# Kernel optimization log

Measured on AMD Instinct MI355X. Metric: run time of the kernel, lower is better.

## Reference

```python
import jax, jax.numpy as jnp
import numpy as np

B, TQ, TK, D = 16, 1024, 4096, 512


def setup_inputs() -> dict:
    key = jax.random.key(0)
    k1, k2, k3 = jax.random.split(key, 3)
    decoder_output = jax.random.normal(k1, (B, TQ, D), dtype=jnp.float32)
    encoder_output = jax.random.normal(k2, (B, TK, D), dtype=jnp.float32)
    # Keras Dense(lstm_size): kernel [D, D] (glorot-ish scale), bias [D] (zeros init)
    W_a = jax.random.normal(k3, (D, D), dtype=jnp.float32) * (1.0 / np.sqrt(D))
    b_a = jnp.zeros((D,), dtype=jnp.float32)
    return {"decoder_output": decoder_output, "encoder_output": encoder_output,
            "W_a": W_a, "b_a": b_a}


def reference(decoder_output, encoder_output, W_a, b_a):
    # Luong 'general' attention:
    # proj = Dense(encoder_output)            [B, Tk, D]
    proj = jnp.einsum('bkd,de->bke', encoder_output, W_a) + b_a
    # score = dec @ proj^T                    [B, Tq, Tk]
    score = jnp.einsum('bqd,bkd->bqk', decoder_output, proj)
    # softmax over encoder time axis (tf axis=2 == last axis here)
    alignment_vector = jax.nn.softmax(score, axis=-1)
    # context = align @ encoder_output        [B, Tq, D]
    context_vector = jnp.einsum('bqk,bkd->bqd', alignment_vector, encoder_output)
    return (context_vector, alignment_vector)
```

## Files before the change

kernel.cpp:

```cpp
#include <hip/hip_runtime.h>
#include <hip/hip_bf16.h>

#define B_  16
#define TQ_ 1024
#define TK_ 4096
#define D_  512

typedef unsigned short u16;
typedef __attribute__((ext_vector_type(8))) short short8;
typedef __attribute__((ext_vector_type(8))) _Float16 f16x8;
typedef __attribute__((ext_vector_type(4))) float f32x4;

__device__ __forceinline__ u16 bf16_rne(float x) {
  unsigned u = __float_as_uint(x);
  u += 0x7FFFu + ((u >> 16) & 1u);
  return (u16)(u >> 16);
}
__device__ __forceinline__ float bf16_as_f32(u16 h) {
  return __uint_as_float(((unsigned)h) << 16);
}
__device__ __forceinline__ void split_bf16(float x, u16& h, u16& l) {
  u16 hh = bf16_rne(x);
  h = hh;
  l = bf16_rne(x - bf16_as_f32(hh));
}

__device__ __forceinline__ void glld16(const void* g, void* lds) {
  __builtin_amdgcn_global_load_lds(
      (const __attribute__((address_space(1))) unsigned int*)g,
      (__attribute__((address_space(3))) unsigned int*)lds, 16, 0, 0);
}

__device__ __forceinline__ int seg_src(int l) {
  return (l & 3) ^ ((l >> 2) & 3) ^ ((l >> 4) & 3);
}

__global__ __launch_bounds__(256) void transpose_conv_kernel(
    const float* __restrict__ E, _Float16* __restrict__ ET,
    _Float16* __restrict__ EF)
{
  __shared__ float tile[64][65];
  const int b  = blockIdx.z;
  const int k0 = blockIdx.x * 64;
  const int d0 = blockIdx.y * 64;
  const float* Eb = E + (long long)b * TK_ * D_;
  _Float16* ETb = ET + (long long)b * D_ * TK_;

  const int t  = threadIdx.x;
  const int r  = t >> 2;
  const int c4 = (t & 3) * 16;

  __align__(16) _Float16 g[16];
  #pragma unroll
  for (int i = 0; i < 16; i += 4) {
    float4 v = *(const float4*)&Eb[(long long)(k0 + r) * D_ + d0 + c4 + i];
    tile[r][c4 + i + 0] = v.x;
    tile[r][c4 + i + 1] = v.y;
    tile[r][c4 + i + 2] = v.z;
    tile[r][c4 + i + 3] = v.w;
    g[i + 0] = (_Float16)v.x;
    g[i + 1] = (_Float16)v.y;
    g[i + 2] = (_Float16)v.z;
    g[i + 3] = (_Float16)v.w;
  }
  if (EF) {
    _Float16* EFb = EF + (long long)b * TK_ * D_;
    uint4* dstF = (uint4*)&EFb[(long long)(k0 + r) * D_ + d0 + c4];
    dstF[0] = ((const uint4*)g)[0];
    dstF[1] = ((const uint4*)g)[1];
  }
  __syncthreads();

  __align__(16) _Float16 h[16];
  #pragma unroll
  for (int i = 0; i < 16; ++i) h[i] = (_Float16)tile[c4 + i][r];
  uint4* dst = (uint4*)&ETb[(long long)(d0 + r) * TK_ + k0 + c4];
  dst[0] = ((const uint4*)h)[0];
  dst[1] = ((const uint4*)h)[1];
}

#define DBM 128
#define DBN 128
#define DBK 32
#define DPAD 40

__global__ __launch_bounds__(256) void gemm_dec2_kernel(
    const float* __restrict__ A, const float* __restrict__ Bm,
    _Float16* __restrict__ Ch, _Float16* __restrict__ Cl)
{
  __shared__ u16 Ah[DBM * DPAD];
  __shared__ u16 Al[DBM * DPAD];
  __shared__ u16 Bh[DBN * DPAD];
  __shared__ u16 Bl[DBN * DPAD];

  const float* Ab = A  + (long long)(blockIdx.y * DBM) * D_;
  const float* Bb = Bm + (long long)(blockIdx.x * DBN) * D_;

  const int t    = threadIdx.x;
  const int r    = t >> 1;
  const int hf   = t & 1;
  const int lane = t & 63;
  const int wave = t >> 6;
  const int wr   = (wave >> 1) * 64;
  const int wc   = (wave & 1) * 64;
  const int ln   = lane & 15;
  const int qd   = lane >> 4;

  f32x4 acc[4][4];
  #pragma unroll
  for (int i = 0; i < 4; ++i)
    #pragma unroll
    for (int j = 0; j < 4; ++j) { f32x4 z = {0.f,0.f,0.f,0.f}; acc[i][j] = z; }

  const float* srcA = Ab + (long long)r * D_ + hf * 16;
  const float* srcB = Bb + (long long)r * D_ + hf * 16;
  u16* dAh = &Ah[r * DPAD + hf * 16];
  u16* dAl = &Al[r * DPAD + hf * 16];
  u16* dBh = &Bh[r * DPAD + hf * 16];
  u16* dBl = &Bl[r * DPAD + hf * 16];

  for (int k0 = 0; k0 < D_; k0 += DBK) {
    {
      __align__(16) u16 h[16], l[16];
      #pragma unroll
      for (int i = 0; i < 16; i += 4) {
        float4 v = *(const float4*)(srcA + k0 + i);
        split_bf16(v.x, h[i+0], l[i+0]);
        split_bf16(v.y, h[i+1], l[i+1]);
        split_bf16(v.z, h[i+2], l[i+2]);
        split_bf16(v.w, h[i+3], l[i+3]);
      }
      ((uint4*)dAh)[0] = ((const uint4*)h)[0];
      ((uint4*)dAh)[1] = ((const uint4*)h)[1];
      ((uint4*)dAl)[0] = ((const uint4*)l)[0];
      ((uint4*)dAl)[1] = ((const uint4*)l)[1];
      #pragma unroll
      for (int i = 0; i < 16; i += 4) {
        float4 v = *(const float4*)(srcB + k0 + i);
        split_bf16(v.x, h[i+0], l[i+0]);
        split_bf16(v.y, h[i+1], l[i+1]);
        split_bf16(v.z, h[i+2], l[i+2]);
        split_bf16(v.w, h[i+3], l[i+3]);
      }
      ((uint4*)dBh)[0] = ((const uint4*)h)[0];
      ((uint4*)dBh)[1] = ((const uint4*)h)[1];
      ((uint4*)dBl)[0] = ((const uint4*)l)[0];
      ((uint4*)dBl)[1] = ((const uint4*)l)[1];
    }
    __syncthreads();

    short8 fah[4], fal[4], fbh[4], fbl[4];
    #pragma unroll
    for (int i = 0; i < 4; ++i) {
      int ra = (wr + i * 16 + ln) * DPAD + qd * 8;
      int rb = (wc + i * 16 + ln) * DPAD + qd * 8;
      fah[i] = *(const short8*)&Ah[ra];
      fal[i] = *(const short8*)&Al[ra];
      fbh[i] = *(const short8*)&Bh[rb];
      fbl[i] = *(const short8*)&Bl[rb];
    }
    #pragma unroll
    for (int i = 0; i < 4; ++i)
      #pragma unroll
      for (int j = 0; j < 4; ++j) {
        acc[i][j] = __builtin_amdgcn_mfma_f32_16x16x32_bf16(fah[i], fbh[j], acc[i][j], 0, 0, 0);
        acc[i][j] = __builtin_amdgcn_mfma_f32_16x16x32_bf16(fah[i], fbl[j], acc[i][j], 0, 0, 0);
        acc[i][j] = __builtin_amdgcn_mfma_f32_16x16x32_bf16(fal[i], fbh[j], acc[i][j], 0, 0, 0);
      }
    __syncthreads();
  }

  const int m0 = blockIdx.y * DBM;
  const int n0 = blockIdx.x * DBN;
  #pragma unroll
  for (int i = 0; i < 4; ++i)
    #pragma unroll
    for (int j = 0; j < 4; ++j)
      #pragma unroll
      for (int rg = 0; rg < 4; ++rg) {
        int row = m0 + wr + i * 16 + qd * 4 + rg;
        int col = n0 + wc + j * 16 + ln;
        float x = acc[i][j][rg];
        _Float16 h = (_Float16)x;
        _Float16 l = (_Float16)(x - (float)h);
        long long idx = (long long)row * D_ + col;
        Ch[idx] = h;
        Cl[idx] = l;
      }
}

#define SBM 128
#define SBN 128
#define SBK 32

template<bool F16B>
__global__ __launch_bounds__(256) void gemm_score_kernel(
    const _Float16* __restrict__ A_h, const _Float16* __restrict__ A_l,
    const float* __restrict__ Bf, const _Float16* __restrict__ B16,
    float* __restrict__ C)
{
  __shared__ _Float16 sAh[SBM * SBK];
  __shared__ _Float16 sAl[SBM * SBK];
  __shared__ _Float16 sB [SBN * SBK];

  const int bz = blockIdx.z;
  const int m0 = blockIdx.y * SBM;
  const int n0 = blockIdx.x * SBN;
  const _Float16* Ahb = A_h + (long long)bz * TQ_ * D_ + (long long)m0 * D_;
  const _Float16* Alb = A_l + (long long)bz * TQ_ * D_ + (long long)m0 * D_;

  const int t    = threadIdx.x;
  const int lane = t & 63;
  const int wave = t >> 6;
  const int wr   = (wave >> 1) * 64;
  const int wc   = (wave & 1) * 64;
  const int ln   = lane & 15;
  const int qd   = lane >> 4;
  const int sw   = qd ^ (ln & 3) ^ (ln >> 2);

  f32x4 acc[4][4];
  #pragma unroll
  for (int i = 0; i < 4; ++i)
    #pragma unroll
    for (int j = 0; j < 4; ++j) { f32x4 z = {0.f,0.f,0.f,0.f}; acc[i][j] = z; }

  const int c0   = wave * 2;
  const int arow = c0 * 16 + (lane >> 2);
  const int ab   = seg_src(lane) * 16;
  const char* gAh = (const char*)Ahb + (long long)arow * D_ * 2 + ab;
  const char* gAl = (const char*)Alb + (long long)arow * D_ * 2 + ab;
  const long long rstep = (long long)16 * D_ * 2;
  char* lAh = (char*)sAh + c0 * 1024 + lane * 16;
  char* lAl = (char*)sAl + c0 * 1024 + lane * 16;
  char* lB  = (char*)sB  + c0 * 1024 + lane * 16;

  const char* gB16 = nullptr;
  if constexpr (F16B) {
    const _Float16* Bb16 = B16 + (long long)bz * TK_ * D_ + (long long)n0 * D_;
    gB16 = (const char*)Bb16 + (long long)arow * D_ * 2 + ab;
  }

  const float* Bb = Bf + (long long)bz * TK_ * D_ + (long long)n0 * D_;
  const int brow = t >> 1;
  const int bhf  = t & 1;
  const float* srcB = Bb + (long long)brow * D_ + bhf * 16;
  const int bh2 = (brow & 3) ^ ((brow >> 2) & 3);
  _Float16* dB0 = &sB[brow * SBK + ((2 * bhf    ) ^ bh2) * 8];
  _Float16* dB1 = &sB[brow * SBK + ((2 * bhf + 1) ^ bh2) * 8];

  for (int k0 = 0; k0 < D_; k0 += SBK) {
    glld16(gAh + (long long)k0 * 2, lAh);
    glld16(gAh + (long long)k0 * 2 + rstep, lAh + 1024);
    glld16(gAl + (long long)k0 * 2, lAl);
    glld16(gAl + (long long)k0 * 2 + rstep, lAl + 1024);
    if constexpr (F16B) {
      glld16(gB16 + (long long)k0 * 2, lB);
      glld16(gB16 + (long long)k0 * 2 + rstep, lB + 1024);
    } else {
      __align__(16) _Float16 hb[16];
      #pragma unroll
      for (int i = 0; i < 16; i += 4) {
        float4 v = *(const float4*)(srcB + k0 + i);
        hb[i+0] = (_Float16)v.x;
        hb[i+1] = (_Float16)v.y;
        hb[i+2] = (_Float16)v.z;
        hb[i+3] = (_Float16)v.w;
      }
      *(uint4*)dB0 = ((const uint4*)hb)[0];
      *(uint4*)dB1 = ((const uint4*)hb)[1];
    }
    __syncthreads();

    f16x8 fah[4], fal[4], fb[4];
    #pragma unroll
    for (int i = 0; i < 4; ++i) {
      int ra = (wr + i * 16 + ln) * SBK + sw * 8;
      int rb = (wc + i * 16 + ln) * SBK + sw * 8;
      fah[i] = *(const f16x8*)&sAh[ra];
      fal[i] = *(const f16x8*)&sAl[ra];
      fb[i]  = *(const f16x8*)&sB[rb];
    }
    #pragma unroll
    for (int i = 0; i < 4; ++i)
      #pragma unroll
      for (int j = 0; j < 4; ++j) {
        acc[i][j] = __builtin_amdgcn_mfma_f32_16x16x32_f16(fah[i], fb[j], acc[i][j], 0, 0, 0);
        acc[i][j] = __builtin_amdgcn_mfma_f32_16x16x32_f16(fal[i], fb[j], acc[i][j], 0, 0, 0);
      }
    __syncthreads();
  }

  float* Cb = C + (long long)bz * TQ_ * TK_;
  #pragma unroll
  for (int i = 0; i < 4; ++i)
    #pragma unroll
    for (int j = 0; j < 4; ++j)
      #pragma unroll
      for (int rg = 0; rg < 4; ++rg) {
        int row = m0 + wr + i * 16 + qd * 4 + rg;
        int col = n0 + wc + j * 16 + ln;
        Cb[(long long)row * TK_ + col] = acc[i][j][rg];
      }
}

template<bool WP16>
__global__ __launch_bounds__(256) void softmax_kernel(
    float* __restrict__ P, _Float16* __restrict__ P16)
{
  __shared__ float red[8];
  float* p = P + (long long)blockIdx.x * TK_;
  const int t    = threadIdx.x;
  const int lane = t & 63;
  const int wave = t >> 6;

  float4 v[4];
  float mx = -3.0e38f;
  #pragma unroll
  for (int i = 0; i < 4; ++i) {
    v[i] = *(const float4*)&p[i * 1024 + t * 4];
    mx = fmaxf(mx, fmaxf(fmaxf(v[i].x, v[i].y), fmaxf(v[i].z, v[i].w)));
  }
  #pragma unroll
  for (int o = 32; o > 0; o >>= 1) mx = fmaxf(mx, __shfl_xor(mx, o, 64));
  if (lane == 0) red[wave] = mx;
  __syncthreads();
  mx = fmaxf(fmaxf(red[0], red[1]), fmaxf(red[2], red[3]));

  float s = 0.f;
  #pragma unroll
  for (int i = 0; i < 4; ++i) {
    v[i].x = __expf(v[i].x - mx);
    v[i].y = __expf(v[i].y - mx);
    v[i].z = __expf(v[i].z - mx);
    v[i].w = __expf(v[i].w - mx);
    s += (v[i].x + v[i].y) + (v[i].z + v[i].w);
  }
  #pragma unroll
  for (int o = 32; o > 0; o >>= 1) s += __shfl_xor(s, o, 64);
  if (lane == 0) red[4 + wave] = s;
  __syncthreads();
  s = (red[4] + red[5]) + (red[6] + red[7]);
  const float inv = 1.0f / s;

  _Float16* p16 = WP16 ? (P16 + (long long)blockIdx.x * TK_) : nullptr;
  #pragma unroll
  for (int i = 0; i < 4; ++i) {
    v[i].x *= inv; v[i].y *= inv; v[i].z *= inv; v[i].w *= inv;
    *(float4*)&p[i * 1024 + t * 4] = v[i];
    if constexpr (WP16) {
      union { _Float16 h[4]; uint2 u; } pk;
      pk.h[0] = (_Float16)v[i].x;
      pk.h[1] = (_Float16)v[i].y;
      pk.h[2] = (_Float16)v[i].z;
      pk.h[3] = (_Float16)v[i].w;
      *(uint2*)&p16[i * 1024 + t * 4] = pk.u;
    }
  }
}

#define CBM 64
#define CBN 256
#define CBK 32

template<bool F16A>
__global__ __launch_bounds__(512) void gemm_ctx_kernel(
    const float* __restrict__ P, const _Float16* __restrict__ P16,
    const _Float16* __restrict__ ET, float* __restrict__ C)
{
  __shared__ _Float16 sA[CBM * CBK];
  __shared__ _Float16 sB[CBN * CBK];

  const int bz = blockIdx.z;
  const int m0 = blockIdx.y * CBM;
  const int n0 = blockIdx.x * CBN;
  const float*    Pb = P  + (long long)bz * TQ_ * TK_ + (long long)m0 * TK_;
  const _Float16* Eb = ET + (long long)bz * D_ * TK_  + (long long)n0 * TK_;

  const int t    = threadIdx.x;
  const int lane = t & 63;
  const int wave = t >> 6;
  const int wr   = (wave >> 2) * 32;
  const int wc   = (wave & 3) * 64;
  const int ln   = lane & 15;
  const int qd   = lane >> 4;
  const int sw   = qd ^ (ln & 3) ^ (ln >> 2);

  f32x4 acc[2][4];
  #pragma unroll
  for (int i = 0; i < 2; ++i)
    #pragma unroll
    for (int j = 0; j < 4; ++j) { f32x4 z = {0.f,0.f,0.f,0.f}; acc[i][j] = z; }

  const int c0   = wave * 2;
  const int brow = c0 * 16 + (lane >> 2);
  const int bb   = seg_src(lane) * 16;
  const char* gB = (const char*)Eb + (long long)brow * TK_ * 2 + bb;
  const long long rstep = (long long)16 * TK_ * 2;
  char* lB = (char*)sB + c0 * 1024 + lane * 16;

  const char* gA16 = nullptr;
  char* lA16 = nullptr;
  if constexpr (F16A) {
    const _Float16* Pb16 = P16 + (long long)bz * TQ_ * TK_ + (long long)m0 * TK_;
    const int acrow = wave * 16 + (lane >> 2);
    gA16 = (const char*)Pb16 + (long long)acrow * TK_ * 2 + bb;
    lA16 = (char*)sA + wave * 1024 + lane * 16;
  }
  const int arow = t >> 3;
  const int aseg = t & 7;
  const float* gA = Pb + (long long)arow * TK_ + aseg * 4;
  const int ah2 = (arow & 3) ^ ((arow >> 2) & 3);
  _Float16* lA = &sA[arow * CBK + (((aseg >> 1) ^ ah2) * 8) + (aseg & 1) * 4];

  for (int k0 = 0; k0 < TK_; k0 += CBK) {
    glld16(gB + (long long)k0 * 2, lB);
    glld16(gB + (long long)k0 * 2 + rstep, lB + 1024);
    if constexpr (F16A) {
      if (wave < 4) glld16(gA16 + (long long)k0 * 2, lA16);
    } else {
      float4 v = *(const float4*)(gA + k0);
      union { _Float16 h[4]; uint2 u; } pk;
      pk.h[0] = (_Float16)v.x;
      pk.h[1] = (_Float16)v.y;
      pk.h[2] = (_Float16)v.z;
      pk.h[3] = (_Float16)v.w;
      *(uint2*)lA = pk.u;
    }
    __syncthreads();

    f16x8 fa[2], fb[4];
    #pragma unroll
    for (int i = 0; i < 2; ++i)
      fa[i] = *(const f16x8*)&sA[(wr + i * 16 + ln) * CBK + sw * 8];
    #pragma unroll
    for (int j = 0; j < 4; ++j)
      fb[j] = *(const f16x8*)&sB[(wc + j * 16 + ln) * CBK + sw * 8];
    #pragma unroll
    for (int i = 0; i < 2; ++i)
      #pragma unroll
      for (int j = 0; j < 4; ++j)
        acc[i][j] = __builtin_amdgcn_mfma_f32_16x16x32_f16(fa[i], fb[j], acc[i][j], 0, 0, 0);
    __syncthreads();
  }

  float* Cb = C + (long long)bz * TQ_ * D_;
  #pragma unroll
  for (int i = 0; i < 2; ++i)
    #pragma unroll
    for (int j = 0; j < 4; ++j)
      #pragma unroll
      for (int rg = 0; rg < 4; ++rg) {
        int row = m0 + wr + i * 16 + qd * 4 + rg;
        int col = n0 + wc + j * 16 + ln;
        Cb[(long long)row * D_ + col] = acc[i][j][rg];
      }
}

extern "C" void kernel_launch(void* const* d_in, const int* in_sizes, int n_in,
                              void* d_out, int out_size, void* d_ws, size_t ws_size,
                              hipStream_t stream) {
  (void)in_sizes; (void)n_in; (void)out_size;
  const float* dec = (const float*)d_in[0];
  const float* enc = (const float*)d_in[1];
  const float* Wa  = (const float*)d_in[2];

  float* ctx   = (float*)d_out;
  float* align = ctx + (long long)B_ * TQ_ * D_;

  char* ws = (char*)d_ws;
  const size_t SZ_ENCT = (size_t)B_ * D_ * TK_ * 2;
  const size_t SZ_DEC2 = (size_t)B_ * TQ_ * D_ * 2;
  const size_t SZ_ENCF = (size_t)B_ * TK_ * D_ * 2;
  const size_t SZ_P16  = (size_t)B_ * TQ_ * TK_ * 2;

  _Float16* encT  = (_Float16*)(ws);
  _Float16* dec2h = (_Float16*)(ws + SZ_ENCT);
  _Float16* dec2l = (_Float16*)(ws + SZ_ENCT + SZ_DEC2);
  _Float16* encF  = (_Float16*)(ws + SZ_ENCT + 2 * SZ_DEC2);
  _Float16* p16   = (_Float16*)(ws + SZ_ENCT);

  const bool mid  = ws_size >= SZ_ENCT + 2 * SZ_DEC2 + SZ_ENCF;
  const bool full = ws_size >= SZ_ENCT + SZ_P16;

  transpose_conv_kernel<<<dim3(TK_ / 64, D_ / 64, B_), 256, 0, stream>>>(
      enc, encT, mid ? encF : nullptr);

  gemm_dec2_kernel<<<dim3(D_ / DBN, (B_ * TQ_) / DBM, 1), 256, 0, stream>>>(
      dec, Wa, dec2h, dec2l);

  if (mid)
    gemm_score_kernel<true><<<dim3(TK_ / SBN, TQ_ / SBM, B_), 256, 0, stream>>>(
        dec2h, dec2l, enc, encF, align);
  else
    gemm_score_kernel<false><<<dim3(TK_ / SBN, TQ_ / SBM, B_), 256, 0, stream>>>(
        dec2h, dec2l, enc, nullptr, align);

  if (full)
    softmax_kernel<true><<<B_ * TQ_, 256, 0, stream>>>(align, p16);
  else
    softmax_kernel<false><<<B_ * TQ_, 256, 0, stream>>>(align, nullptr);

  if (full)
    gemm_ctx_kernel<true><<<dim3(D_ / CBN, TQ_ / CBM, B_), 512, 0, stream>>>(
        align, p16, encT, ctx);
  else
    gemm_ctx_kernel<false><<<dim3(D_ / CBN, TQ_ / CBM, B_), 512, 0, stream>>>(
        align, nullptr, encT, ctx);
}
```

Baseline: 866.4 us.

## Double-buffer LDS in score and context GEMMs, widen ctx K-tile, remap ctx blocks

Both the score GEMM and the context GEMM now use two LDS buffers per operand. The next K-tile is staged while MFMAs run on the current one, which drops one barrier per iteration. The context GEMM also doubles its K tile to 64 with a new XOR swizzle, and flattens the grid into a 1D launch with a remapping meant to spread batches and tiles across XCDs for better L2 locality. The cost is twice the LDS per block, which may lower occupancy, and more complex index math.

```diff
diff --git a/kernel.cpp b/kernel.cpp
--- a/kernel.cpp
+++ b/kernel.cpp
@@ -31,7 +31,7 @@
       (__attribute__((address_space(3))) unsigned int*)lds, 16, 0, 0);
 }
 
-__device__ __forceinline__ int seg_src(int l) {
+__device__ __forceinline__ int seg_src4(int l) {
   return (l & 3) ^ ((l >> 2) & 3) ^ ((l >> 4) & 3);
 }
 
@@ -192,6 +192,7 @@
 #define SBM 128
 #define SBN 128
 #define SBK 32
+#define S_NT (D_ / SBK)
 
 template<bool F16B>
 __global__ __launch_bounds__(256) void gemm_score_kernel(
@@ -199,9 +200,9 @@
     const float* __restrict__ Bf, const _Float16* __restrict__ B16,
     float* __restrict__ C)
 {
-  __shared__ _Float16 sAh[SBM * SBK];
-  __shared__ _Float16 sAl[SBM * SBK];
-  __shared__ _Float16 sB [SBN * SBK];
+  __shared__ _Float16 sAh[2][SBM * SBK];
+  __shared__ _Float16 sAl[2][SBM * SBK];
+  __shared__ _Float16 sB [2][SBN * SBK];
 
   const int bz = blockIdx.z;
   const int m0 = blockIdx.y * SBM;
@@ -226,13 +227,11 @@
 
   const int c0   = wave * 2;
   const int arow = c0 * 16 + (lane >> 2);
-  const int ab   = seg_src(lane) * 16;
+  const int ab   = seg_src4(lane) * 16;
   const char* gAh = (const char*)Ahb + (long long)arow * D_ * 2 + ab;
   const char* gAl = (const char*)Alb + (long long)arow * D_ * 2 + ab;
   const long long rstep = (long long)16 * D_ * 2;
-  char* lAh = (char*)sAh + c0 * 1024 + lane * 16;
-  char* lAl = (char*)sAl + c0 * 1024 + lane * 16;
-  char* lB  = (char*)sB  + c0 * 1024 + lane * 16;
+  const int dstoff = c0 * 1024 + lane * 16;
 
   const char* gB16 = nullptr;
   if constexpr (F16B) {
@@ -245,17 +244,21 @@
   const int bhf  = t & 1;
   const float* srcB = Bb + (long long)brow * D_ + bhf * 16;
   const int bh2 = (brow & 3) ^ ((brow >> 2) & 3);
-  _Float16* dB0 = &sB[brow * SBK + ((2 * bhf    ) ^ bh2) * 8];
-  _Float16* dB1 = &sB[brow * SBK + ((2 * bhf + 1) ^ bh2) * 8];
-
-  for (int k0 = 0; k0 < D_; k0 += SBK) {
-    glld16(gAh + (long long)k0 * 2, lAh);
-    glld16(gAh + (long long)k0 * 2 + rstep, lAh + 1024);
-    glld16(gAl + (long long)k0 * 2, lAl);
-    glld16(gAl + (long long)k0 * 2 + rstep, lAl + 1024);
+  const int db0 = brow * SBK + ((2 * bhf    ) ^ bh2) * 8;
+  const int db1 = brow * SBK + ((2 * bhf + 1) ^ bh2) * 8;
+
+  auto stage = [&](int buf, int k0) {
+    const long long ko = (long long)k0 * 2;
+    char* dAh = (char*)sAh[buf] + dstoff;
+    char* dAl = (char*)sAl[buf] + dstoff;
+    glld16(gAh + ko, dAh);
+    glld16(gAh + ko + rstep, dAh + 1024);
+    glld16(gAl + ko, dAl);
+    glld16(gAl + ko + rstep, dAl + 1024);
     if constexpr (F16B) {
-      glld16(gB16 + (long long)k0 * 2, lB);
-      glld16(gB16 + (long long)k0 * 2 + rstep, lB + 1024);
+      char* dBv = (char*)sB[buf] + dstoff;
+      glld16(gB16 + ko, dBv);
+      glld16(gB16 + ko + rstep, dBv + 1024);
     } else {
       __align__(16) _Float16 hb[16];
       #pragma unroll
@@ -266,19 +269,29 @@
         hb[i+2] = (_Float16)v.z;
         hb[i+3] = (_Float16)v.w;
       }
-      *(uint4*)dB0 = ((const uint4*)hb)[0];
-      *(uint4*)dB1 = ((const uint4*)hb)[1];
+      *(uint4*)&sB[buf][db0] = ((const uint4*)hb)[0];
+      *(uint4*)&sB[buf][db1] = ((const uint4*)hb)[1];
     }
-    __syncthreads();
-
+  };
+
+  stage(0, 0);
+  __syncthreads();
+
+  int cur = 0;
+  for (int tt = 0; tt < S_NT; ++tt) {
+    if (tt + 1 < S_NT) stage(cur ^ 1, (tt + 1) * SBK);
+
+    const _Float16* bAh = sAh[cur];
+    const _Float16* bAl = sAl[cur];
+    const _Float16* bBv = sB[cur];
     f16x8 fah[4], fal[4], fb[4];
     #pragma unroll
     for (int i = 0; i < 4; ++i) {
       int ra = (wr + i * 16 + ln) * SBK + sw * 8;
       int rb = (wc + i * 16 + ln) * SBK + sw * 8;
-      fah[i] = *(const f16x8*)&sAh[ra];
-      fal[i] = *(const f16x8*)&sAl[ra];
-      fb[i]  = *(const f16x8*)&sB[rb];
+      fah[i] = *(const f16x8*)&bAh[ra];
+      fal[i] = *(const f16x8*)&bAl[ra];
+      fb[i]  = *(const f16x8*)&bBv[rb];
     }
     #pragma unroll
     for (int i = 0; i < 4; ++i)
@@ -288,6 +301,7 @@
         acc[i][j] = __builtin_amdgcn_mfma_f32_16x16x32_f16(fal[i], fb[j], acc[i][j], 0, 0, 0);
       }
     __syncthreads();
+    cur ^= 1;
   }
 
   float* Cb = C + (long long)bz * TQ_ * TK_;
@@ -360,19 +374,23 @@
 
 #define CBM 64
 #define CBN 256
-#define CBK 32
+#define CBK 64
+#define C_NT (TK_ / CBK)
 
 template<bool F16A>
 __global__ __launch_bounds__(512) void gemm_ctx_kernel(
     const float* __restrict__ P, const _Float16* __restrict__ P16,
     const _Float16* __restrict__ ET, float* __restrict__ C)
 {
-  __shared__ _Float16 sA[CBM * CBK];
-  __shared__ _Float16 sB[CBN * CBK];
-
-  const int bz = blockIdx.z;
-  const int m0 = blockIdx.y * CBM;
-  const int n0 = blockIdx.x * CBN;
+  __shared__ _Float16 sA[2][CBM * CBK];
+  __shared__ _Float16 sB[2][CBN * CBK];
+
+  const int bid = blockIdx.x;
+  const int s   = (bid & 7) * 64 + (bid >> 3);
+  const int m0  = (s & 15) * CBM;
+  const int n0  = ((s >> 4) & 1) * CBN;
+  const int bz  = s >> 5;
+
   const float*    Pb = P  + (long long)bz * TQ_ * TK_ + (long long)m0 * TK_;
   const _Float16* Eb = ET + (long long)bz * D_ * TK_  + (long long)n0 * TK_;
 
@@ -383,7 +401,7 @@
   const int wc   = (wave & 3) * 64;
   const int ln   = lane & 15;
   const int qd   = lane >> 4;
-  const int sw   = qd ^ (ln & 3) ^ (ln >> 2);
+  const int l7   = ln & 7;
 
   f32x4 acc[2][4];
   #pragma unroll
@@ -391,56 +409,72 @@
     #pragma unroll
     for (int j = 0; j < 4; ++j) { f32x4 z = {0.f,0.f,0.f,0.f}; acc[i][j] = z; }
 
-  const int c0   = wave * 2;
-  const int brow = c0 * 16 + (lane >> 2);
-  const int bb   = seg_src(lane) * 16;
-  const char* gB = (const char*)Eb + (long long)brow * TK_ * 2 + bb;
-  const long long rstep = (long long)16 * TK_ * 2;
-  char* lB = (char*)sB + c0 * 1024 + lane * 16;
-
+  const int l8   = lane >> 3;
+  const int sseg = (lane & 7) ^ l8;
+  const char* gB = (const char*)Eb + ((long long)(wave * 32 + l8) * TK_) * 2 + sseg * 16;
+  const long long bstep = (long long)8 * TK_ * 2;
+  const int bdst = wave * 4096 + lane * 16;
   const char* gA16 = nullptr;
-  char* lA16 = nullptr;
   if constexpr (F16A) {
     const _Float16* Pb16 = P16 + (long long)bz * TQ_ * TK_ + (long long)m0 * TK_;
-    const int acrow = wave * 16 + (lane >> 2);
-    gA16 = (const char*)Pb16 + (long long)acrow * TK_ * 2 + bb;
-    lA16 = (char*)sA + wave * 1024 + lane * 16;
-  }
-  const int arow = t >> 3;
-  const int aseg = t & 7;
-  const float* gA = Pb + (long long)arow * TK_ + aseg * 4;
-  const int ah2 = (arow & 3) ^ ((arow >> 2) & 3);
-  _Float16* lA = &sA[arow * CBK + (((aseg >> 1) ^ ah2) * 8) + (aseg & 1) * 4];
-
-  for (int k0 = 0; k0 < TK_; k0 += CBK) {
-    glld16(gB + (long long)k0 * 2, lB);
-    glld16(gB + (long long)k0 * 2 + rstep, lB + 1024);
+    gA16 = (const char*)Pb16 + ((long long)(wave * 8 + l8) * TK_) * 2 + sseg * 16;
+  }
+  const int adst = wave * 1024 + lane * 16;
+
+  const int arowf = t >> 3;
+  const int asegf = t & 7;
+  const float* gAf = Pb + (long long)arowf * TK_ + asegf * 8;
+  const int afoff = arowf * CBK + ((asegf ^ (arowf & 7)) * 8);
+
+  auto stage = [&](int buf, int k0) {
+    const long long ko = (long long)k0 * 2;
+    char* dB = (char*)sB[buf] + bdst;
+    #pragma unroll
+    for (int j = 0; j < 4; ++j)
+      glld16(gB + ko + j * bstep, dB + j * 1024);
     if constexpr (F16A) {
-      if (wave < 4) glld16(gA16 + (long long)k0 * 2, lA16);
+      glld16(gA16 + ko, (char*)sA[buf] + adst);
     } else {
-      float4 v = *(const float4*)(gA + k0);
-      union { _Float16 h[4]; uint2 u; } pk;
-      pk.h[0] = (_Float16)v.x;
-      pk.h[1] = (_Float16)v.y;
-      pk.h[2] = (_Float16)v.z;
-      pk.h[3] = (_Float16)v.w;
-      *(uint2*)lA = pk.u;
+      float4 v0 = *(const float4*)(gAf + k0);
+      float4 v1 = *(const float4*)(gAf + k0 + 4);
+      __align__(16) _Float16 hb[8];
+      hb[0] = (_Float16)v0.x; hb[1] = (_Float16)v0.y;
+      hb[2] = (_Float16)v0.z; hb[3] = (_Float16)v0.w;
+      hb[4] = (_Float16)v1.x; hb[5] = (_Float16)v1.y;
+      hb[6] = (_Float16)v1.z; hb[7] = (_Float16)v1.w;
+      *(uint4*)&sA[buf][afoff] = *(const uint4*)hb;
     }
+  };
+
+  stage(0, 0);
+  __syncthreads();
+
+  int cur = 0;
+  for (int tt = 0; tt < C_NT; ++tt) {
+    if (tt + 1 < C_NT) stage(cur ^ 1, (tt + 1) * CBK);
+
+    const _Float16* bA  = sA[cur];
+    const _Float16* bBv = sB[cur];
+    f16x8 fa[2][2], fb[4][2];
+    #pragma unroll
+    for (int i = 0; i < 2; ++i)
+      #pragma unroll
+      for (int kk = 0; kk < 2; ++kk)
+        fa[i][kk] = *(const f16x8*)&bA[(wr + i * 16 + ln) * CBK + (((kk * 4 + qd) ^ l7) * 8)];
+    #pragma unroll
+    for (int j = 0; j < 4; ++j)
+      #pragma unroll
+      for (int kk = 0; kk < 2; ++kk)
+        fb[j][kk] = *(const f16x8*)&bBv[(wc + j * 16 + ln) * CBK + (((kk * 4 + qd) ^ l7) * 8)];
+    #pragma unroll
+    for (int i = 0; i < 2; ++i)
+      #pragma unroll
+      for (int j = 0; j < 4; ++j)
+        #pragma unroll
+        for (int kk = 0; kk < 2; ++kk)
+          acc[i][j] = __builtin_amdgcn_mfma_f32_16x16x32_f16(fa[i][kk], fb[j][kk], acc[i][j], 0, 0, 0);
     __syncthreads();
-
-    f16x8 fa[2], fb[4];
-    #pragma unroll
-    for (int i = 0; i < 2; ++i)
-      fa[i] = *(const f16x8*)&sA[(wr + i * 16 + ln) * CBK + sw * 8];
-    #pragma unroll
-    for (int j = 0; j < 4; ++j)
-      fb[j] = *(const f16x8*)&sB[(wc + j * 16 + ln) * CBK + sw * 8];
-    #pragma unroll
-    for (int i = 0; i < 2; ++i)
-      #pragma unroll
-      for (int j = 0; j < 4; ++j)
-        acc[i][j] = __builtin_amdgcn_mfma_f32_16x16x32_f16(fa[i], fb[j], acc[i][j], 0, 0, 0);
-    __syncthreads();
+    cur ^= 1;
   }
 
   float* Cb = C + (long long)bz * TQ_ * D_;
@@ -501,9 +535,9 @@
     softmax_kernel<false><<<B_ * TQ_, 256, 0, stream>>>(align, nullptr);
 
   if (full)
-    gemm_ctx_kernel<true><<<dim3(D_ / CBN, TQ_ / CBM, B_), 512, 0, stream>>>(
+    gemm_ctx_kernel<true><<<dim3((TQ_ / CBM) * (D_ / CBN) * B_), 512, 0, stream>>>(
         align, p16, encT, ctx);
   else
-    gemm_ctx_kernel<false><<<dim3(D_ / CBN, TQ_ / CBM, B_), 512, 0, stream>>>(
+    gemm_ctx_kernel<false><<<dim3((TQ_ / CBM) * (D_ / CBN) * B_), 512, 0, stream>>>(
         align, nullptr, encT, ctx);
 }
```

Result: faster. 848.1 us (-2.1%).
